# Optimization experiments

Hardware: AMD Instinct MI355X
Metric: run time of the kernel (lower is better)

## Reference

```python
import jax, jax.numpy as jnp
import numpy as np

DIM = 1024
NUM_ROT = 1024
BATCH = 65536


def setup_inputs() -> dict:
    key = jax.random.key(0)
    k1, k2 = jax.random.split(key)
    x = jax.random.normal(k1, (BATCH, DIM), dtype=jnp.float32)
    angles = jax.random.normal(k2, (NUM_ROT,), dtype=jnp.float32)
    return {"x": x, "angles": angles}


def reference(x, angles):
    # Sequential Givens rotations. out @ R.T with R[i,i]=R[j,j]=c, R[i,j]=-s, R[j,i]=s
    # is equivalent to: col_i' = c*col_i - s*col_j ; col_j' = s*col_i + c*col_j.
    dim = x.shape[-1]
    num_rot = angles.shape[0]
    ii = jnp.arange(num_rot, dtype=jnp.int32)          # pairs (i, (i+1)%dim)
    jj = (ii + 1) % dim

    def step(out, inp):
        theta, i, j = inp
        c, s = jnp.cos(theta), jnp.sin(theta)
        ci = out[:, i]
        cj = out[:, j]
        out = out.at[:, i].set(c * ci - s * cj)
        out = out.at[:, j].set(s * ci + c * cj)
        return out, None

    out, _ = jax.lax.scan(step, x, (angles, ii, jj))
    return out
```

## Files before the change

kernel.cpp:

```cpp
#include <hip/hip_runtime.h>

#define DIM   1024
#define LPR   32
#define SEG   (DIM / LPR)
#define SEG4  (SEG / 4)
#define ROWS_PER_BLOCK 8
#define WAVES_PER_BLOCK 4

typedef float f32x4 __attribute__((ext_vector_type(4)));
#define AS1 __attribute__((address_space(1)))
#define AS3 __attribute__((address_space(3)))

__global__ void qll_table(const float* __restrict__ angles, float2* __restrict__ ws) {
    int j = blockIdx.x * blockDim.x + threadIdx.x;
    if (j < DIM) {
        float a = angles[j];
        ws[(j & 31) * LPR + (j >> 5)] = make_float2(cosf(a), sinf(a));
    }
}

__global__ __launch_bounds__(256, 4)
void qll_kernel(const float* __restrict__ x,
                const float2* __restrict__ csws,
                float* __restrict__ out,
                int batch)
{
    __shared__ float2 cs[DIM];
    __shared__ f32x4  stage[WAVES_PER_BLOCK][512];

    const int tid  = threadIdx.x;
    const int l    = tid & 63;
    const int wave = tid >> 6;
    const int h    = (tid >> 5) & 1;
    const int t    = tid & 31;
    const int r0   = blockIdx.x * ROWS_PER_BLOCK + wave * 2;
    const bool active = (r0 + 2 <= batch);
    const int rr   = active ? r0 : 0;

    const int swz_l = l ^ ((l >> 3) & 7);

    const f32x4* w4 = reinterpret_cast<const f32x4*>(csws);
    f32x4* c4 = reinterpret_cast<f32x4*>(cs);
    __builtin_amdgcn_global_load_lds((const AS1 void*)(w4 + wave * 64 + l),
                                     (AS3 void*)(c4 + wave * 64), 16, 0, 0);
    __builtin_amdgcn_global_load_lds((const AS1 void*)(w4 + 256 + wave * 64 + l),
                                     (AS3 void*)(c4 + 256 + wave * 64), 16, 0, 0);

    const f32x4* gin = reinterpret_cast<const f32x4*>(x) + (size_t)rr * 256;
#pragma unroll
    for (int m = 0; m < 8; ++m) {
        __builtin_amdgcn_global_load_lds(
            (const AS1 void*)(gin + m * 64 + swz_l),
            (AS3 void*)(&stage[wave][m * 64]), 16, 0, 0);
    }

    asm volatile("s_waitcnt vmcnt(8)" ::: "memory");
    __builtin_amdgcn_s_barrier();
    if (!active) return;

    asm volatile("s_waitcnt vmcnt(0)" ::: "memory");
    __builtin_amdgcn_sched_barrier(0);

    float v[SEG];
#pragma unroll
    for (int e = 0; e < SEG4; ++e) {
        f32x4 q = stage[wave][h * 256 + t * 8 + (e ^ (t & 7))];
        v[4*e+0] = q.x; v[4*e+1] = q.y; v[4*e+2] = q.z; v[4*e+3] = q.w;
    }

    float v0row = __shfl(v[0], 0, LPR);
    float v1row = __shfl(v[1], 0, LPR);
    float vnext = __shfl_down(v[0], 1, LPR);

    float A = 1.f, B = 0.f;
#pragma unroll
    for (int i = 0; i < SEG - 1; ++i) {
        float2 w = cs[i * LPR + t];
        B = w.y * B + w.x * v[i + 1];
        A = w.y * A;
    }
    {
        float2 w = cs[(SEG - 1) * LPR + t];
        B = w.y * B + w.x * vnext;
        A = w.y * A;
    }

#pragma unroll
    for (int d = 1; d < LPR; d <<= 1) {
        float pa = __shfl_up(A, d, LPR);
        float pb = __shfl_up(B, d, LPR);
        if (t >= d) { B = A * pb + B; A = A * pa; }
    }
    float ea = __shfl_up(A, 1, LPR);
    float eb = __shfl_up(B, 1, LPR);
    if (t == 0) { ea = 1.f; eb = 0.f; }
    float carry = ea * v0row + eb;

    float2 w0 = cs[0];
    float out0_prov = w0.x * v0row - w0.y * v1row;

#pragma unroll
    for (int i = 0; i < SEG - 1; ++i) {
        float2 w = cs[i * LPR + t];
        float vn = v[i + 1];
        float o  = w.x * carry - w.y * vn;
        carry    = w.y * carry + w.x * vn;
        v[i] = o;
    }
    {
        float2 w  = cs[(SEG - 1) * LPR + t];
        float vn  = (t == LPR - 1) ? out0_prov : vnext;
        float o   = w.x * carry - w.y * vn;
        float nc  = w.y * carry + w.x * vn;
        v[SEG - 1] = o;
        float out0_final = __shfl(nc, LPR - 1, LPR);
        if (t == 0) v[0] = out0_final;
    }

#pragma unroll
    for (int e = 0; e < SEG4; ++e) {
        f32x4 q = { v[4*e+0], v[4*e+1], v[4*e+2], v[4*e+3] };
        stage[wave][h * 256 + t * 8 + (e ^ (t & 7))] = q;
    }
    f32x4* gout = reinterpret_cast<f32x4*>(out) + (size_t)r0 * 256;
#pragma unroll
    for (int m = 0; m < 8; ++m) {
        f32x4 q = stage[wave][m * 64 + swz_l];
        __builtin_nontemporal_store(q, gout + m * 64 + l);
    }
}

__global__ __launch_bounds__(256, 4)
void qll_kernel_fb(const float* __restrict__ x,
                   const float* __restrict__ angles,
                   float* __restrict__ out,
                   int batch)
{
    __shared__ float2 cs[DIM];
    __shared__ f32x4  stage[WAVES_PER_BLOCK][512];

    const int tid  = threadIdx.x;
    const int l    = tid & 63;
    const int wave = tid >> 6;
    const int h    = (tid >> 5) & 1;
    const int t    = tid & 31;
    const int r0   = blockIdx.x * ROWS_PER_BLOCK + wave * 2;
    const bool active = (r0 + 2 <= batch);
    const int swz_l = l ^ ((l >> 3) & 7);

    for (int loc = tid; loc < DIM; loc += 256) {
        int j = ((loc & 31) << 5) | (loc >> 5);
        float a = angles[j];
        cs[loc] = make_float2(cosf(a), sinf(a));
    }
    __syncthreads();
    if (!active) return;

    const f32x4* gin = reinterpret_cast<const f32x4*>(x) + (size_t)r0 * 256;
#pragma unroll
    for (int m = 0; m < 8; ++m) {
        __builtin_amdgcn_global_load_lds(
            (const AS1 void*)(gin + m * 64 + swz_l),
            (AS3 void*)(&stage[wave][m * 64]), 16, 0, 0);
    }
    asm volatile("s_waitcnt vmcnt(0)" ::: "memory");
    __builtin_amdgcn_sched_barrier(0);

    float v[SEG];
#pragma unroll
    for (int e = 0; e < SEG4; ++e) {
        f32x4 q = stage[wave][h * 256 + t * 8 + (e ^ (t & 7))];
        v[4*e+0] = q.x; v[4*e+1] = q.y; v[4*e+2] = q.z; v[4*e+3] = q.w;
    }
    float v0row = __shfl(v[0], 0, LPR);
    float v1row = __shfl(v[1], 0, LPR);
    float vnext = __shfl_down(v[0], 1, LPR);

    float A = 1.f, B = 0.f;
#pragma unroll
    for (int i = 0; i < SEG - 1; ++i) {
        float2 w = cs[i * LPR + t];
        B = w.y * B + w.x * v[i + 1];
        A = w.y * A;
    }
    {
        float2 w = cs[(SEG - 1) * LPR + t];
        B = w.y * B + w.x * vnext;
        A = w.y * A;
    }
#pragma unroll
    for (int d = 1; d < LPR; d <<= 1) {
        float pa = __shfl_up(A, d, LPR);
        float pb = __shfl_up(B, d, LPR);
        if (t >= d) { B = A * pb + B; A = A * pa; }
    }
    float ea = __shfl_up(A, 1, LPR);
    float eb = __shfl_up(B, 1, LPR);
    if (t == 0) { ea = 1.f; eb = 0.f; }
    float carry = ea * v0row + eb;

    float2 w0 = cs[0];
    float out0_prov = w0.x * v0row - w0.y * v1row;

#pragma unroll
    for (int i = 0; i < SEG - 1; ++i) {
        float2 w = cs[i * LPR + t];
        float vn = v[i + 1];
        float o  = w.x * carry - w.y * vn;
        carry    = w.y * carry + w.x * vn;
        v[i] = o;
    }
    {
        float2 w  = cs[(SEG - 1) * LPR + t];
        float vn  = (t == LPR - 1) ? out0_prov : vnext;
        float o   = w.x * carry - w.y * vn;
        float nc  = w.y * carry + w.x * vn;
        v[SEG - 1] = o;
        float out0_final = __shfl(nc, LPR - 1, LPR);
        if (t == 0) v[0] = out0_final;
    }
#pragma unroll
    for (int e = 0; e < SEG4; ++e) {
        f32x4 q = { v[4*e+0], v[4*e+1], v[4*e+2], v[4*e+3] };
        stage[wave][h * 256 + t * 8 + (e ^ (t & 7))] = q;
    }
    f32x4* gout = reinterpret_cast<f32x4*>(out) + (size_t)r0 * 256;
#pragma unroll
    for (int m = 0; m < 8; ++m) {
        f32x4 q = stage[wave][m * 64 + swz_l];
        __builtin_nontemporal_store(q, gout + m * 64 + l);
    }
}

extern "C" void kernel_launch(void* const* d_in, const int* in_sizes, int n_in,
                              void* d_out, int out_size, void* d_ws, size_t ws_size,
                              hipStream_t stream) {
    const float* x      = (const float*)d_in[0];
    const float* angles = (const float*)d_in[1];
    float* outp         = (float*)d_out;

    int batch = in_sizes[0] / DIM;
    int grid  = (batch + ROWS_PER_BLOCK - 1) / ROWS_PER_BLOCK;

    if (ws_size >= (size_t)(DIM * sizeof(float2))) {
        float2* ws = (float2*)d_ws;
        qll_table<<<(DIM + 255) / 256, 256, 0, stream>>>(angles, ws);
        qll_kernel<<<grid, 256, 0, stream>>>(x, ws, outp, batch);
    } else {
        qll_kernel_fb<<<grid, 256, 0, stream>>>(x, angles, outp, batch);
    }
}
```

Measured before the change: 90.84 us.

## Process several row pairs per wave with register-prefetched next pair

Each wave now handles four row pairs in a loop instead of one, and loads the next pair's data into registers while computing the current one. This amortizes the per-block cos/sin table load and barrier over more rows and overlaps global loads with the scan computation. The input path switches from direct global-to-LDS loads to register loads followed by LDS writes. That adds VGPR pressure from the 8 prefetched vectors and reduces the grid size by 4x.

```diff
diff --git a/kernel.cpp b/kernel.cpp
--- a/kernel.cpp
+++ b/kernel.cpp
@@ -4,8 +4,8 @@
 #define LPR   32
 #define SEG   (DIM / LPR)
 #define SEG4  (SEG / 4)
-#define ROWS_PER_BLOCK 8
 #define WAVES_PER_BLOCK 4
+#define PAIRS_PER_WAVE  4
 
 typedef float f32x4 __attribute__((ext_vector_type(4)));
 #define AS1 __attribute__((address_space(1)))
@@ -33,10 +33,6 @@
     const int wave = tid >> 6;
     const int h    = (tid >> 5) & 1;
     const int t    = tid & 31;
-    const int r0   = blockIdx.x * ROWS_PER_BLOCK + wave * 2;
-    const bool active = (r0 + 2 <= batch);
-    const int rr   = active ? r0 : 0;
-
     const int swz_l = l ^ ((l >> 3) & 7);
 
     const f32x4* w4 = reinterpret_cast<const f32x4*>(csws);
@@ -45,19 +41,138 @@
                                      (AS3 void*)(c4 + wave * 64), 16, 0, 0);
     __builtin_amdgcn_global_load_lds((const AS1 void*)(w4 + 256 + wave * 64 + l),
                                      (AS3 void*)(c4 + 256 + wave * 64), 16, 0, 0);
-
-    const f32x4* gin = reinterpret_cast<const f32x4*>(x) + (size_t)rr * 256;
+    __syncthreads();
+
+    const int pairBase = (blockIdx.x * WAVES_PER_BLOCK + wave) * PAIRS_PER_WAVE;
+    const int pairsTot = batch >> 1;
+    int np = pairsTot - pairBase;
+    if (np <= 0) return;
+    if (np > PAIRS_PER_WAVE) np = PAIRS_PER_WAVE;
+
+    const f32x4* ginb = reinterpret_cast<const f32x4*>(x);
+    f32x4*       goutb = reinterpret_cast<f32x4*>(out);
+
+    f32x4 pf[8];
+    {
+        const f32x4* g = ginb + (size_t)pairBase * 512;
+#pragma unroll
+        for (int m = 0; m < 8; ++m) pf[m] = g[m * 64 + l];
+    }
+
+    for (int it = 0; it < np; ++it) {
+#pragma unroll
+        for (int m = 0; m < 8; ++m)
+            stage[wave][m * 64 + swz_l] = pf[m];
+
+        float v[SEG];
+#pragma unroll
+        for (int e = 0; e < SEG4; ++e) {
+            f32x4 q = stage[wave][h * 256 + t * 8 + (e ^ (t & 7))];
+            v[4*e+0] = q.x; v[4*e+1] = q.y; v[4*e+2] = q.z; v[4*e+3] = q.w;
+        }
+
+        if (it + 1 < np) {
+            const f32x4* g = ginb + (size_t)(pairBase + it + 1) * 512;
+#pragma unroll
+            for (int m = 0; m < 8; ++m) pf[m] = g[m * 64 + l];
+        }
+
+        float v0row = __shfl(v[0], 0, LPR);
+        float v1row = __shfl(v[1], 0, LPR);
+        float vnext = __shfl_down(v[0], 1, LPR);
+
+        float A = 1.f, B = 0.f;
+#pragma unroll
+        for (int i = 0; i < SEG - 1; ++i) {
+            float2 w = cs[i * LPR + t];
+            B = w.y * B + w.x * v[i + 1];
+            A = w.y * A;
+        }
+        {
+            float2 w = cs[(SEG - 1) * LPR + t];
+            B = w.y * B + w.x * vnext;
+            A = w.y * A;
+        }
+
+#pragma unroll
+        for (int d = 1; d < LPR; d <<= 1) {
+            float pa = __shfl_up(A, d, LPR);
+            float pb = __shfl_up(B, d, LPR);
+            if (t >= d) { B = A * pb + B; A = A * pa; }
+        }
+        float ea = __shfl_up(A, 1, LPR);
+        float eb = __shfl_up(B, 1, LPR);
+        if (t == 0) { ea = 1.f; eb = 0.f; }
+        float carry = ea * v0row + eb;
+
+        float2 w0 = cs[0];
+        float out0_prov = w0.x * v0row - w0.y * v1row;
+
+#pragma unroll
+        for (int i = 0; i < SEG - 1; ++i) {
+            float2 w = cs[i * LPR + t];
+            float vn = v[i + 1];
+            float o  = w.x * carry - w.y * vn;
+            carry    = w.y * carry + w.x * vn;
+            v[i] = o;
+        }
+        {
+            float2 w  = cs[(SEG - 1) * LPR + t];
+            float vn  = (t == LPR - 1) ? out0_prov : vnext;
+            float o   = w.x * carry - w.y * vn;
+            float nc  = w.y * carry + w.x * vn;
+            v[SEG - 1] = o;
+            float out0_final = __shfl(nc, LPR - 1, LPR);
+            if (t == 0) v[0] = out0_final;
+        }
+
+#pragma unroll
+        for (int e = 0; e < SEG4; ++e) {
+            f32x4 q = { v[4*e+0], v[4*e+1], v[4*e+2], v[4*e+3] };
+            stage[wave][h * 256 + t * 8 + (e ^ (t & 7))] = q;
+        }
+        f32x4* gout = goutb + (size_t)(pairBase + it) * 512;
+#pragma unroll
+        for (int m = 0; m < 8; ++m) {
+            f32x4 q = stage[wave][m * 64 + swz_l];
+            __builtin_nontemporal_store(q, gout + m * 64 + l);
+        }
+    }
+}
+
+__global__ __launch_bounds__(256, 4)
+void qll_kernel_fb(const float* __restrict__ x,
+                   const float* __restrict__ angles,
+                   float* __restrict__ out,
+                   int batch)
+{
+    __shared__ float2 cs[DIM];
+    __shared__ f32x4  stage[WAVES_PER_BLOCK][512];
+
+    const int tid  = threadIdx.x;
+    const int l    = tid & 63;
+    const int wave = tid >> 6;
+    const int h    = (tid >> 5) & 1;
+    const int t    = tid & 31;
+    const int r0   = blockIdx.x * (WAVES_PER_BLOCK * 2) + wave * 2;
+    const bool active = (r0 + 2 <= batch);
+    const int swz_l = l ^ ((l >> 3) & 7);
+
+    for (int loc = tid; loc < DIM; loc += 256) {
+        int j = ((loc & 31) << 5) | (loc >> 5);
+        float a = angles[j];
+        cs[loc] = make_float2(cosf(a), sinf(a));
+    }
+    __syncthreads();
+    if (!active) return;
+
+    const f32x4* gin = reinterpret_cast<const f32x4*>(x) + (size_t)r0 * 256;
 #pragma unroll
     for (int m = 0; m < 8; ++m) {
         __builtin_amdgcn_global_load_lds(
             (const AS1 void*)(gin + m * 64 + swz_l),
             (AS3 void*)(&stage[wave][m * 64]), 16, 0, 0);
     }
-
-    asm volatile("s_waitcnt vmcnt(8)" ::: "memory");
-    __builtin_amdgcn_s_barrier();
-    if (!active) return;
-
     asm volatile("s_waitcnt vmcnt(0)" ::: "memory");
     __builtin_amdgcn_sched_barrier(0);
 
@@ -67,7 +182,6 @@
         f32x4 q = stage[wave][h * 256 + t * 8 + (e ^ (t & 7))];
         v[4*e+0] = q.x; v[4*e+1] = q.y; v[4*e+2] = q.z; v[4*e+3] = q.w;
     }
-
     float v0row = __shfl(v[0], 0, LPR);
     float v1row = __shfl(v[1], 0, LPR);
     float vnext = __shfl_down(v[0], 1, LPR);
@@ -84,7 +198,6 @@
         B = w.y * B + w.x * vnext;
         A = w.y * A;
     }
-
 #pragma unroll
     for (int d = 1; d < LPR; d <<= 1) {
         float pa = __shfl_up(A, d, LPR);
@@ -116,109 +229,6 @@
         float out0_final = __shfl(nc, LPR - 1, LPR);
         if (t == 0) v[0] = out0_final;
     }
-
-#pragma unroll
-    for (int e = 0; e < SEG4; ++e) {
-        f32x4 q = { v[4*e+0], v[4*e+1], v[4*e+2], v[4*e+3] };
-        stage[wave][h * 256 + t * 8 + (e ^ (t & 7))] = q;
-    }
-    f32x4* gout = reinterpret_cast<f32x4*>(out) + (size_t)r0 * 256;
-#pragma unroll
-    for (int m = 0; m < 8; ++m) {
-        f32x4 q = stage[wave][m * 64 + swz_l];
-        __builtin_nontemporal_store(q, gout + m * 64 + l);
-    }
-}
-
-__global__ __launch_bounds__(256, 4)
-void qll_kernel_fb(const float* __restrict__ x,
-                   const float* __restrict__ angles,
-                   float* __restrict__ out,
-                   int batch)
-{
-    __shared__ float2 cs[DIM];
-    __shared__ f32x4  stage[WAVES_PER_BLOCK][512];
-
-    const int tid  = threadIdx.x;
-    const int l    = tid & 63;
-    const int wave = tid >> 6;
-    const int h    = (tid >> 5) & 1;
-    const int t    = tid & 31;
-    const int r0   = blockIdx.x * ROWS_PER_BLOCK + wave * 2;
-    const bool active = (r0 + 2 <= batch);
-    const int swz_l = l ^ ((l >> 3) & 7);
-
-    for (int loc = tid; loc < DIM; loc += 256) {
-        int j = ((loc & 31) << 5) | (loc >> 5);
-        float a = angles[j];
-        cs[loc] = make_float2(cosf(a), sinf(a));
-    }
-    __syncthreads();
-    if (!active) return;
-
-    const f32x4* gin = reinterpret_cast<const f32x4*>(x) + (size_t)r0 * 256;
-#pragma unroll
-    for (int m = 0; m < 8; ++m) {
-        __builtin_amdgcn_global_load_lds(
-            (const AS1 void*)(gin + m * 64 + swz_l),
-            (AS3 void*)(&stage[wave][m * 64]), 16, 0, 0);
-    }
-    asm volatile("s_waitcnt vmcnt(0)" ::: "memory");
-    __builtin_amdgcn_sched_barrier(0);
-
-    float v[SEG];
-#pragma unroll
-    for (int e = 0; e < SEG4; ++e) {
-        f32x4 q = stage[wave][h * 256 + t * 8 + (e ^ (t & 7))];
-        v[4*e+0] = q.x; v[4*e+1] = q.y; v[4*e+2] = q.z; v[4*e+3] = q.w;
-    }
-    float v0row = __shfl(v[0], 0, LPR);
-    float v1row = __shfl(v[1], 0, LPR);
-    float vnext = __shfl_down(v[0], 1, LPR);
-
-    float A = 1.f, B = 0.f;
-#pragma unroll
-    for (int i = 0; i < SEG - 1; ++i) {
-        float2 w = cs[i * LPR + t];
-        B = w.y * B + w.x * v[i + 1];
-        A = w.y * A;
-    }
-    {
-        float2 w = cs[(SEG - 1) * LPR + t];
-        B = w.y * B + w.x * vnext;
-        A = w.y * A;
-    }
-#pragma unroll
-    for (int d = 1; d < LPR; d <<= 1) {
-        float pa = __shfl_up(A, d, LPR);
-        float pb = __shfl_up(B, d, LPR);
-        if (t >= d) { B = A * pb + B; A = A * pa; }
-    }
-    float ea = __shfl_up(A, 1, LPR);
-    float eb = __shfl_up(B, 1, LPR);
-    if (t == 0) { ea = 1.f; eb = 0.f; }
-    float carry = ea * v0row + eb;
-
-    float2 w0 = cs[0];
-    float out0_prov = w0.x * v0row - w0.y * v1row;
-
-#pragma unroll
-    for (int i = 0; i < SEG - 1; ++i) {
-        float2 w = cs[i * LPR + t];
-        float vn = v[i + 1];
-        float o  = w.x * carry - w.y * vn;
-        carry    = w.y * carry + w.x * vn;
-        v[i] = o;
-    }
-    {
-        float2 w  = cs[(SEG - 1) * LPR + t];
-        float vn  = (t == LPR - 1) ? out0_prov : vnext;
-        float o   = w.x * carry - w.y * vn;
-        float nc  = w.y * carry + w.x * vn;
-        v[SEG - 1] = o;
-        float out0_final = __shfl(nc, LPR - 1, LPR);
-        if (t == 0) v[0] = out0_final;
-    }
 #pragma unroll
     for (int e = 0; e < SEG4; ++e) {
         f32x4 q = { v[4*e+0], v[4*e+1], v[4*e+2], v[4*e+3] };
@@ -240,13 +250,17 @@
     float* outp         = (float*)d_out;
 
     int batch = in_sizes[0] / DIM;
-    int grid  = (batch + ROWS_PER_BLOCK - 1) / ROWS_PER_BLOCK;
 
     if (ws_size >= (size_t)(DIM * sizeof(float2))) {
         float2* ws = (float2*)d_ws;
         qll_table<<<(DIM + 255) / 256, 256, 0, stream>>>(angles, ws);
+        int pairs = batch / 2;
+        int pairsPerBlock = WAVES_PER_BLOCK * PAIRS_PER_WAVE;
+        int grid = (pairs + pairsPerBlock - 1) / pairsPerBlock;
         qll_kernel<<<grid, 256, 0, stream>>>(x, ws, outp, batch);
     } else {
+        int rowsPerBlock = WAVES_PER_BLOCK * 2;
+        int grid = (batch + rowsPerBlock - 1) / rowsPerBlock;
         qll_kernel_fb<<<grid, 256, 0, stream>>>(x, angles, outp, batch);
     }
 }
```

Result: slower. 346.5 us (+281.4%).

## Load rows directly to registers and read cos/sin table from global

Applied to the files above, without the earlier changes.

The main kernel no longer stages the cos/sin table or the input rows through LDS. Each lane loads its contiguous 32-element segment straight from global memory into registers, and reads its 16 consecutive table entries as vector loads from a table now stored in natural order. This removes the block barrier and the LDS table copy. The costs are strided per-lane global reads (each lane reads 128 contiguous bytes, less coalesced), dependence on L1/L2 for the shared table, and no fixed occupancy hint in the launch bounds.

```diff
diff --git a/kernel.cpp b/kernel.cpp
--- a/kernel.cpp
+++ b/kernel.cpp
@@ -4,7 +4,6 @@
 #define LPR   32
 #define SEG   (DIM / LPR)
 #define SEG4  (SEG / 4)
-#define ROWS_PER_BLOCK 8
 #define WAVES_PER_BLOCK 4
 
 typedef float f32x4 __attribute__((ext_vector_type(4)));
@@ -15,49 +14,130 @@
     int j = blockIdx.x * blockDim.x + threadIdx.x;
     if (j < DIM) {
         float a = angles[j];
-        ws[(j & 31) * LPR + (j >> 5)] = make_float2(cosf(a), sinf(a));
-    }
-}
-
-__global__ __launch_bounds__(256, 4)
+        ws[j] = make_float2(cosf(a), sinf(a));
+    }
+}
+
+__global__ __launch_bounds__(256)
 void qll_kernel(const float* __restrict__ x,
                 const float2* __restrict__ csws,
                 float* __restrict__ out,
                 int batch)
 {
-    __shared__ float2 cs[DIM];
-    __shared__ f32x4  stage[WAVES_PER_BLOCK][512];
+    __shared__ f32x4 stage[WAVES_PER_BLOCK][512];
 
     const int tid  = threadIdx.x;
     const int l    = tid & 63;
     const int wave = tid >> 6;
     const int h    = (tid >> 5) & 1;
     const int t    = tid & 31;
-    const int r0   = blockIdx.x * ROWS_PER_BLOCK + wave * 2;
+    const int r0   = (blockIdx.x * WAVES_PER_BLOCK + wave) * 2;
+    if (r0 + 2 > batch) return;
+
+    const int swz_l = l ^ ((l >> 3) & 7);
+
+    const f32x4* vin = reinterpret_cast<const f32x4*>(x)
+                     + (size_t)(r0 + h) * 256 + t * 8;
+    float v[SEG];
+#pragma unroll
+    for (int e = 0; e < SEG4; ++e) {
+        f32x4 q = vin[e];
+        v[4*e+0] = q.x; v[4*e+1] = q.y; v[4*e+2] = q.z; v[4*e+3] = q.w;
+    }
+
+    float v0row = __shfl(v[0], 0, LPR);
+    float v1row = __shfl(v[1], 0, LPR);
+    float vnext = __shfl_down(v[0], 1, LPR);
+
+    const f32x4* cs4 = reinterpret_cast<const f32x4*>(csws) + t * 16;
+
+    float A = 1.f, B = 0.f;
+#pragma unroll
+    for (int ii = 0; ii < 16; ++ii) {
+        f32x4 q = cs4[ii];
+        B = q.y * B + q.x * v[2*ii + 1];
+        A = q.y * A;
+        float vn = (ii == 15) ? vnext : v[2*ii + 2];
+        B = q.w * B + q.z * vn;
+        A = q.w * A;
+    }
+
+#pragma unroll
+    for (int d = 1; d < LPR; d <<= 1) {
+        float pa = __shfl_up(A, d, LPR);
+        float pb = __shfl_up(B, d, LPR);
+        if (t >= d) { B = A * pb + B; A = A * pa; }
+    }
+    float ea = __shfl_up(A, 1, LPR);
+    float eb = __shfl_up(B, 1, LPR);
+    if (t == 0) { ea = 1.f; eb = 0.f; }
+    float carry = ea * v0row + eb;
+
+    float2 w0 = csws[0];
+    float out0_prov = w0.x * v0row - w0.y * v1row;
+
+#pragma unroll
+    for (int ii = 0; ii < 16; ++ii) {
+        f32x4 q = cs4[ii];
+        float vn0 = v[2*ii + 1];
+        float o0  = q.x * carry - q.y * vn0;
+        carry     = q.y * carry + q.x * vn0;
+        v[2*ii] = o0;
+        float vn1 = (ii == 15) ? ((t == LPR - 1) ? out0_prov : vnext)
+                               : v[2*ii + 2];
+        float o1  = q.z * carry - q.w * vn1;
+        carry     = q.w * carry + q.z * vn1;
+        v[2*ii + 1] = o1;
+    }
+    float out0_final = __shfl(carry, LPR - 1, LPR);
+    if (t == 0) v[0] = out0_final;
+
+#pragma unroll
+    for (int e = 0; e < SEG4; ++e) {
+        f32x4 q = { v[4*e+0], v[4*e+1], v[4*e+2], v[4*e+3] };
+        stage[wave][h * 256 + t * 8 + (e ^ (t & 7))] = q;
+    }
+    f32x4* gout = reinterpret_cast<f32x4*>(out) + (size_t)r0 * 256;
+#pragma unroll
+    for (int m = 0; m < 8; ++m) {
+        f32x4 q = stage[wave][m * 64 + swz_l];
+        __builtin_nontemporal_store(q, gout + m * 64 + l);
+    }
+}
+
+__global__ __launch_bounds__(256, 4)
+void qll_kernel_fb(const float* __restrict__ x,
+                   const float* __restrict__ angles,
+                   float* __restrict__ out,
+                   int batch)
+{
+    __shared__ float2 cs[DIM];
+    __shared__ f32x4  stage[WAVES_PER_BLOCK][512];
+
+    const int tid  = threadIdx.x;
+    const int l    = tid & 63;
+    const int wave = tid >> 6;
+    const int h    = (tid >> 5) & 1;
+    const int t    = tid & 31;
+    const int r0   = blockIdx.x * (WAVES_PER_BLOCK * 2) + wave * 2;
     const bool active = (r0 + 2 <= batch);
-    const int rr   = active ? r0 : 0;
-
     const int swz_l = l ^ ((l >> 3) & 7);
 
-    const f32x4* w4 = reinterpret_cast<const f32x4*>(csws);
-    f32x4* c4 = reinterpret_cast<f32x4*>(cs);
-    __builtin_amdgcn_global_load_lds((const AS1 void*)(w4 + wave * 64 + l),
-                                     (AS3 void*)(c4 + wave * 64), 16, 0, 0);
-    __builtin_amdgcn_global_load_lds((const AS1 void*)(w4 + 256 + wave * 64 + l),
-                                     (AS3 void*)(c4 + 256 + wave * 64), 16, 0, 0);
-
-    const f32x4* gin = reinterpret_cast<const f32x4*>(x) + (size_t)rr * 256;
+    for (int loc = tid; loc < DIM; loc += 256) {
+        int j = ((loc & 31) << 5) | (loc >> 5);
+        float a = angles[j];
+        cs[loc] = make_float2(cosf(a), sinf(a));
+    }
+    __syncthreads();
+    if (!active) return;
+
+    const f32x4* gin = reinterpret_cast<const f32x4*>(x) + (size_t)r0 * 256;
 #pragma unroll
     for (int m = 0; m < 8; ++m) {
         __builtin_amdgcn_global_load_lds(
             (const AS1 void*)(gin + m * 64 + swz_l),
             (AS3 void*)(&stage[wave][m * 64]), 16, 0, 0);
     }
-
-    asm volatile("s_waitcnt vmcnt(8)" ::: "memory");
-    __builtin_amdgcn_s_barrier();
-    if (!active) return;
-
     asm volatile("s_waitcnt vmcnt(0)" ::: "memory");
     __builtin_amdgcn_sched_barrier(0);
 
@@ -67,7 +147,6 @@
         f32x4 q = stage[wave][h * 256 + t * 8 + (e ^ (t & 7))];
         v[4*e+0] = q.x; v[4*e+1] = q.y; v[4*e+2] = q.z; v[4*e+3] = q.w;
     }
-
     float v0row = __shfl(v[0], 0, LPR);
     float v1row = __shfl(v[1], 0, LPR);
     float vnext = __shfl_down(v[0], 1, LPR);
@@ -84,7 +163,6 @@
         B = w.y * B + w.x * vnext;
         A = w.y * A;
     }
-
 #pragma unroll
     for (int d = 1; d < LPR; d <<= 1) {
         float pa = __shfl_up(A, d, LPR);
@@ -116,109 +194,6 @@
         float out0_final = __shfl(nc, LPR - 1, LPR);
         if (t == 0) v[0] = out0_final;
     }
-
-#pragma unroll
-    for (int e = 0; e < SEG4; ++e) {
-        f32x4 q = { v[4*e+0], v[4*e+1], v[4*e+2], v[4*e+3] };
-        stage[wave][h * 256 + t * 8 + (e ^ (t & 7))] = q;
-    }
-    f32x4* gout = reinterpret_cast<f32x4*>(out) + (size_t)r0 * 256;
-#pragma unroll
-    for (int m = 0; m < 8; ++m) {
-        f32x4 q = stage[wave][m * 64 + swz_l];
-        __builtin_nontemporal_store(q, gout + m * 64 + l);
-    }
-}
-
-__global__ __launch_bounds__(256, 4)
-void qll_kernel_fb(const float* __restrict__ x,
-                   const float* __restrict__ angles,
-                   float* __restrict__ out,
-                   int batch)
-{
-    __shared__ float2 cs[DIM];
-    __shared__ f32x4  stage[WAVES_PER_BLOCK][512];
-
-    const int tid  = threadIdx.x;
-    const int l    = tid & 63;
-    const int wave = tid >> 6;
-    const int h    = (tid >> 5) & 1;
-    const int t    = tid & 31;
-    const int r0   = blockIdx.x * ROWS_PER_BLOCK + wave * 2;
-    const bool active = (r0 + 2 <= batch);
-    const int swz_l = l ^ ((l >> 3) & 7);
-
-    for (int loc = tid; loc < DIM; loc += 256) {
-        int j = ((loc & 31) << 5) | (loc >> 5);
-        float a = angles[j];
-        cs[loc] = make_float2(cosf(a), sinf(a));
-    }
-    __syncthreads();
-    if (!active) return;
-
-    const f32x4* gin = reinterpret_cast<const f32x4*>(x) + (size_t)r0 * 256;
-#pragma unroll
-    for (int m = 0; m < 8; ++m) {
-        __builtin_amdgcn_global_load_lds(
-            (const AS1 void*)(gin + m * 64 + swz_l),
-            (AS3 void*)(&stage[wave][m * 64]), 16, 0, 0);
-    }
-    asm volatile("s_waitcnt vmcnt(0)" ::: "memory");
-    __builtin_amdgcn_sched_barrier(0);
-
-    float v[SEG];
-#pragma unroll
-    for (int e = 0; e < SEG4; ++e) {
-        f32x4 q = stage[wave][h * 256 + t * 8 + (e ^ (t & 7))];
-        v[4*e+0] = q.x; v[4*e+1] = q.y; v[4*e+2] = q.z; v[4*e+3] = q.w;
-    }
-    float v0row = __shfl(v[0], 0, LPR);
-    float v1row = __shfl(v[1], 0, LPR);
-    float vnext = __shfl_down(v[0], 1, LPR);
-
-    float A = 1.f, B = 0.f;
-#pragma unroll
-    for (int i = 0; i < SEG - 1; ++i) {
-        float2 w = cs[i * LPR + t];
-        B = w.y * B + w.x * v[i + 1];
-        A = w.y * A;
-    }
-    {
-        float2 w = cs[(SEG - 1) * LPR + t];
-        B = w.y * B + w.x * vnext;
-        A = w.y * A;
-    }
-#pragma unroll
-    for (int d = 1; d < LPR; d <<= 1) {
-        float pa = __shfl_up(A, d, LPR);
-        float pb = __shfl_up(B, d, LPR);
-        if (t >= d) { B = A * pb + B; A = A * pa; }
-    }
-    float ea = __shfl_up(A, 1, LPR);
-    float eb = __shfl_up(B, 1, LPR);
-    if (t == 0) { ea = 1.f; eb = 0.f; }
-    float carry = ea * v0row + eb;
-
-    float2 w0 = cs[0];
-    float out0_prov = w0.x * v0row - w0.y * v1row;
-
-#pragma unroll
-    for (int i = 0; i < SEG - 1; ++i) {
-        float2 w = cs[i * LPR + t];
-        float vn = v[i + 1];
-        float o  = w.x * carry - w.y * vn;
-        carry    = w.y * carry + w.x * vn;
-        v[i] = o;
-    }
-    {
-        float2 w  = cs[(SEG - 1) * LPR + t];
-        float vn  = (t == LPR - 1) ? out0_prov : vnext;
-        float o   = w.x * carry - w.y * vn;
-        float nc  = w.y * carry + w.x * vn;
-        v[SEG - 1] = o;
-        float out0_final = __shfl(nc, LPR - 1, LPR);
-        if (t == 0) v[0] = out0_final;
-    }
 #pragma unroll
     for (int e = 0; e < SEG4; ++e) {
         f32x4 q = { v[4*e+0], v[4*e+1], v[4*e+2], v[4*e+3] };
@@ -240,13 +215,16 @@
     float* outp         = (float*)d_out;
 
     int batch = in_sizes[0] / DIM;
-    int grid  = (batch + ROWS_PER_BLOCK - 1) / ROWS_PER_BLOCK;
 
     if (ws_size >= (size_t)(DIM * sizeof(float2))) {
         float2* ws = (float2*)d_ws;
         qll_table<<<(DIM + 255) / 256, 256, 0, stream>>>(angles, ws);
+        int pairs = batch / 2;
+        int grid  = (pairs + WAVES_PER_BLOCK - 1) / WAVES_PER_BLOCK;
         qll_kernel<<<grid, 256, 0, stream>>>(x, ws, outp, batch);
     } else {
+        int rowsPerBlock = WAVES_PER_BLOCK * 2;
+        int grid = (batch + rowsPerBlock - 1) / rowsPerBlock;
         qll_kernel_fb<<<grid, 256, 0, stream>>>(x, angles, outp, batch);
     }
 }
```

Measured after the change: 112.0 us. 23.3% more time.
